# Optimization experiments

Hardware: AMD Instinct MI355X
Metric: run time of the kernel (lower is better)

## Reference

```python
import jax, jax.numpy as jnp
import numpy as np

EPS = 1e-6
B, T, J, D, H = 8, 512, 26, 256, 8
DH = D // H
HID = 4 * D


def logmap0(x):
    # x: [..., d+1] on hyperboloid (curvature -1). Tangent at origin -> [..., d]
    x0 = jnp.clip(x[..., :1], 1.0 + 1e-7, None)
    xs = x[..., 1:]
    n = jnp.maximum(jnp.linalg.norm(xs, axis=-1, keepdims=True), EPS)
    return jnp.arccosh(x0) * xs / n


def expmap0(v):
    # v: [..., d] tangent at origin -> [..., d+1] on hyperboloid
    n = jnp.maximum(jnp.linalg.norm(v, axis=-1, keepdims=True), EPS)
    return jnp.concatenate([jnp.cosh(n), jnp.sinh(n) * v / n], axis=-1)


def layernorm(v, g, b):
    m = jnp.mean(v, axis=-1, keepdims=True)
    var = jnp.var(v, axis=-1, keepdims=True)
    return (v - m) * jax.lax.rsqrt(var + 1e-5) * g + b


def lorentz_residual(x, z):
    # Lorentz centroid: normalize x+z so <m,m>_L = -1
    m = x + z
    mink = -m[..., :1] ** 2 + jnp.sum(m[..., 1:] ** 2, axis=-1, keepdims=True)
    return m / jnp.sqrt(jnp.clip(-mink, EPS, None))


def setup_inputs() -> dict:
    key = jax.random.key(0)
    ks = jax.random.split(key, 12)
    xs = jax.random.normal(ks[0], (B, T, J, D), jnp.float32) * 0.5
    x0 = jnp.sqrt(1.0 + jnp.sum(xs ** 2, axis=-1, keepdims=True))
    x = jnp.concatenate([x0, xs], axis=-1)  # valid points on H^d
    s = 1.0 / np.sqrt(D)
    inp = {
        "x": x,
        "g1": jnp.ones((D,), jnp.float32), "beta1": jnp.zeros((D,), jnp.float32),
        "Wq": jax.random.normal(ks[1], (D, D), jnp.float32) * s,
        "Wk": jax.random.normal(ks[2], (D, D), jnp.float32) * s,
        "Wv": jax.random.normal(ks[3], (D, D), jnp.float32) * s,
        "Wo": jax.random.normal(ks[4], (D, D), jnp.float32) * s,
        "bq": jnp.zeros((D,), jnp.float32), "bk": jnp.zeros((D,), jnp.float32),
        "bv": jnp.zeros((D,), jnp.float32), "bo": jnp.zeros((D,), jnp.float32),
        "g2": jnp.ones((D,), jnp.float32), "beta2": jnp.zeros((D,), jnp.float32),
        "W1": jax.random.normal(ks[5], (D, HID), jnp.float32) * s,
        "bf1": jnp.zeros((HID,), jnp.float32),
        "W2": jax.random.normal(ks[6], (HID, D), jnp.float32) * (1.0 / np.sqrt(HID)),
        "bf2": jnp.zeros((D,), jnp.float32),
    }
    return inp


def reference(x, g1, beta1, Wq, Wk, Wv, Wo, bq, bk, bv, bo, g2, beta2, W1, bf1, W2, bf2):
    # norm1: tangent-space LayerNorm
    u = layernorm(logmap0(x), g1, beta1)            # [B,T,J,D]
    xn = expmap0(u)
    # linear temporal attention (per joint, across T)
    t = logmap0(xn)
    q = (t @ Wq + bq).reshape(B, T, J, H, DH)
    k = (t @ Wk + bk).reshape(B, T, J, H, DH)
    v = (t @ Wv + bv).reshape(B, T, J, H, DH)
    pq = jax.nn.elu(q) + 1.0
    pk = jax.nn.elu(k) + 1.0
    kv = jnp.einsum('btjhk,btjhd->bjhkd', pk, v)    # O(T) global context
    ksum = jnp.sum(pk, axis=1)                      # [B,J,H,DH]
    num = jnp.einsum('btjhk,bjhkd->btjhd', pq, kv)
    den = jnp.einsum('btjhk,bjhk->btjh', pq, ksum)[..., None] + EPS
    o = (num / den).reshape(B, T, J, D) @ Wo + bo
    z = expmap0(o)
    # Lorentz (Minkowski) residual
    h = lorentz_residual(x, z)
    # norm2 + FFN in tangent space
    u2 = layernorm(logmap0(h), g2, beta2)
    f = jax.nn.gelu(u2 @ W1 + bf1) @ W2 + bf2
    return expmap0(f)
```

## Files before the change

kernel.cpp:

```cpp
#include <hip/hip_runtime.h>
#include <hip/hip_bf16.h>
#include <math.h>


#define EPSF 1e-6f
#define B_ 8
#define T_ 512
#define J_ 26
#define D_ 256
#define H_ 8
#define DH_ 32
#define HID_ 1024
#define NP1 257
#define R_ (B_*T_*J_)

typedef float  f32x4  __attribute__((ext_vector_type(4)));
typedef short  s16x8  __attribute__((ext_vector_type(8)));
typedef short  s16x4  __attribute__((ext_vector_type(4)));

__device__ __forceinline__ int rp_to_r(int rp) {
  int bj = rp >> 9, t = rp & 511;
  int b = bj / 26, j = bj - 26 * b;
  return (b * 512 + t) * 26 + j;
}

__device__ __forceinline__ void async16(const void* g, void* l) {
  __builtin_amdgcn_global_load_lds(
      (const __attribute__((address_space(1))) unsigned int*)g,
      (__attribute__((address_space(3))) unsigned int*)l, 16, 0, 0);
}

__device__ __forceinline__ float wave_sum(float v) {
#pragma unroll
  for (int m = 32; m; m >>= 1) v += __shfl_xor(v, m, 64);
  return v;
}

__global__ __launch_bounds__(256) void k_wconv(const float* __restrict__ W,
                                               __hip_bfloat16* __restrict__ Wt,
                                               int K, int N) {
  __shared__ float tile[32][33];
  int n0 = blockIdx.x * 32, k0 = blockIdx.y * 32;
  int tx = threadIdx.x, ty = threadIdx.y;
#pragma unroll
  for (int i = ty; i < 32; i += 8) tile[i][tx] = W[(size_t)(k0 + i) * N + n0 + tx];
  __syncthreads();
#pragma unroll
  for (int i = ty; i < 32; i += 8)
    Wt[(size_t)(n0 + i) * K + k0 + tx] = __float2bfloat16(tile[tx][i]);
}

__global__ __launch_bounds__(256) void k_t(const float* __restrict__ x,
                                           const float* __restrict__ g1,
                                           const float* __restrict__ beta1,
                                           __hip_bfloat16* __restrict__ t) {
  int rp = blockIdx.x * 4 + (threadIdx.x >> 6);
  int l = threadIdx.x & 63;
  int r = rp_to_r(rp);
  const float* xr = x + (size_t)r * NP1;
  float xs[4];
#pragma unroll
  for (int i = 0; i < 4; ++i) xs[i] = xr[1 + l + 64*i];
  float p1 = xs[0]+xs[1]+xs[2]+xs[3];
  float p2 = xs[0]*xs[0]+xs[1]*xs[1]+xs[2]*xs[2]+xs[3]*xs[3];
  float s1 = wave_sum(p1);
  float s2 = wave_sum(p2);
  float mean = s1 * (1.0f/256.0f);
  float var = s2 * (1.0f/256.0f) - mean*mean;
  float rstd = rsqrtf(var + 1e-5f);
#pragma unroll
  for (int i = 0; i < 4; ++i) {
    int c = l + 64*i;
    t[(size_t)rp * D_ + c] = __float2bfloat16((xs[i]-mean)*rstd*g1[c] + beta1[c]);
  }
}

#define PHASE(BUF, MH, NH, GIDX, DO_VM) {                                      \
    s16x8 af_[4][2]; s16x8 bf_[2][2];                                          \
    const char* ab_ = lds + ((BUF)*2+(MH))*16384;                              \
    const char* bb_ = lds + 65536 + ((BUF)*2+(NH))*16384;                      \
    _Pragma("unroll") for (int f_ = 0; f_ < 4; ++f_)                           \
      _Pragma("unroll") for (int ks_ = 0; ks_ < 2; ++ks_)                      \
        af_[f_][ks_] = *(const s16x8*)(ab_ + aoffs[f_][ks_]);                  \
    _Pragma("unroll") for (int ni_ = 0; ni_ < 2; ++ni_)                        \
      _Pragma("unroll") for (int ks_ = 0; ks_ < 2; ++ks_)                      \
        bf_[ni_][ks_] = *(const s16x8*)(bb_ + boffs[ni_][ks_]);                \
    STAGE_HALF((GIDX) + 6);                                                    \
    if (DO_VM) asm volatile("s_waitcnt vmcnt(4)" ::: "memory");                \
    asm volatile("s_barrier" ::: "memory");                                    \
    __builtin_amdgcn_sched_barrier(0);                                         \
    __builtin_amdgcn_s_setprio(1);                                             \
    _Pragma("unroll") for (int ks_ = 0; ks_ < 2; ++ks_)                        \
      _Pragma("unroll") for (int f_ = 0; f_ < 4; ++f_)                         \
        _Pragma("unroll") for (int ni_ = 0; ni_ < 2; ++ni_)                    \
          acc[(MH)*4+f_][(NH)*2+ni_] = __builtin_amdgcn_mfma_f32_16x16x32_bf16(\
              bf_[ni_][ks_], af_[f_][ks_], acc[(MH)*4+f_][(NH)*2+ni_], 0,0,0); \
    __builtin_amdgcn_s_setprio(0);                                             \
    asm volatile("s_barrier" ::: "memory");                                    \
  }

template<int ACT, int OUTF, int KDIM>
__global__ __launch_bounds__(512, 2) void k_gemm(const __hip_bfloat16* __restrict__ A,
                                                 const __hip_bfloat16* __restrict__ Bt,
                                                 const float* __restrict__ bias,
                                                 void* __restrict__ Cout,
                                                 int M, int N) {
  extern __shared__ char lds[];
  constexpr int NKT = KDIM / 64;
  int tid = threadIdx.x;
  int w = tid >> 6, l = tid & 63;
  int wr = w >> 2, wc = w & 3;
  int ml = l & 15, quad = l >> 4;
  int n0 = blockIdx.x * 256, m0 = blockIdx.y * 256;

  const short* Ag = (const short*)A + (size_t)m0 * KDIM;
  const short* Bg = (const short*)Bt + (size_t)n0 * KDIM;

  int srow = w*8 + (l >> 3);
  int scol = (((l & 7) ^ ((l >> 3) & 7)) * 8);

  auto STAGE_HALF = [&](int n) {
    if (n >= 4*NKT) return;
    int kt = n >> 2;
    int isB = n & 1, h = (n >> 1) & 1, buf = kt & 1;
    const short* src = isB ? Bg : Ag;
    const short* g0 = src + (size_t)(h*128 + srow) * KDIM + kt*64 + scol;
    char* dst = lds + isB*65536 + (buf*2 + h)*16384 + w*1024;
    async16(g0, dst);
    async16(g0 + (size_t)64 * KDIM, dst + 8192);
  };

  int aoffs[4][2], boffs[2][2];
#pragma unroll
  for (int f = 0; f < 4; ++f) {
    int r = wr*64 + f*16 + ml;
#pragma unroll
    for (int ks = 0; ks < 2; ++ks)
      aoffs[f][ks] = (r*128 + ks*64 + quad*16) ^ ((ml & 7) << 4);
  }
#pragma unroll
  for (int ni = 0; ni < 2; ++ni) {
    int rb = wc*32 + ni*16 + ml;
#pragma unroll
    for (int ks = 0; ks < 2; ++ks)
      boffs[ni][ks] = (rb*128 + ks*64 + quad*16) ^ ((ml & 7) << 4);
  }

  f32x4 acc[8][4];
#pragma unroll
  for (int i = 0; i < 8; ++i)
#pragma unroll
    for (int j = 0; j < 4; ++j) acc[i][j] = {0.f, 0.f, 0.f, 0.f};

#pragma unroll
  for (int n = 0; n < 6; ++n) STAGE_HALF(n);
  asm volatile("s_waitcnt vmcnt(4)" ::: "memory");
  asm volatile("s_barrier" ::: "memory");

  for (int cc = 0; cc < NKT/2; ++cc) {
    int g0 = cc * 8;
    PHASE(0, 0, 0, g0+0, 0)
    PHASE(0, 0, 1, g0+1, 0)
    PHASE(0, 1, 0, g0+2, 0)
    PHASE(0, 1, 1, g0+3, 1)
    PHASE(1, 0, 0, g0+4, 0)
    PHASE(1, 0, 1, g0+5, 0)
    PHASE(1, 1, 0, g0+6, 0)
    PHASE(1, 1, 1, g0+7, 1)
  }

#pragma unroll
  for (int mi = 0; mi < 8; ++mi) {
    size_t row = (size_t)(m0 + (mi>>2)*128 + wr*64 + (mi&3)*16 + ml);
#pragma unroll
    for (int nj = 0; nj < 4; ++nj) {
      int col = n0 + (nj>>1)*128 + wc*32 + (nj&1)*16 + quad*4;
      f32x4 bj = *(const f32x4*)&bias[col];
      f32x4 v = acc[mi][nj] + bj;
      if (ACT == 1) {
#pragma unroll
        for (int e = 0; e < 4; ++e) v[e] = (v[e] > 0.0f) ? v[e] + 1.0f : __expf(v[e]);
      } else if (ACT == 2) {
#pragma unroll
        for (int e = 0; e < 4; ++e) {
          float vv = v[e], v2 = vv * vv;
          float ex = __expf(vv * fmaf(v2, -0.0713548327f, -1.5957691216f));
          v[e] = vv * __builtin_amdgcn_rcpf(1.0f + ex);
        }
      }
      if (OUTF) {
        *(f32x4*)&((float*)Cout)[row * N + col] = v;
      } else {
        s16x4 sv;
#pragma unroll
        for (int e = 0; e < 4; ++e) {
          __hip_bfloat16 b = __float2bfloat16(v[e]);
          sv[e] = *(short*)&b;
        }
        *(s16x4*)&((__hip_bfloat16*)Cout)[row * N + col] = sv;
      }
    }
  }
}

__global__ __launch_bounds__(256) void k_kv(const __hip_bfloat16* __restrict__ pk,
                                            const __hip_bfloat16* __restrict__ v,
                                            float* __restrict__ kv,
                                            float* __restrict__ ksum) {
  __shared__ float spk[2][64*36];
  __shared__ float sv [2][64*33];
  __shared__ float sks[8][32];
  int blk = blockIdx.x;
  int h = blk & 7, bj = blk >> 3;
  int tid = threadIdx.x;
  int tq = tid >> 2;
  int qc = tid & 3;
  int kgrp = tid >> 5;
  int dd = tid & 31;

  const short* pkg = (const short*)pk + (size_t)bj * 512 * 256 + h*32 + qc*8;
  const short* vg  = (const short*)v  + (size_t)bj * 512 * 256 + h*32 + qc*8;

  float acc[4] = {0.f, 0.f, 0.f, 0.f};
  float ks = 0.f;
  s16x8 rp_, rv_;

  auto GLOAD = [&](int c) {
    size_t off = (size_t)(c*64 + tq) * 256;
    rp_ = *(const s16x8*)(pkg + off);
    rv_ = *(const s16x8*)(vg + off);
  };
  auto DSWRITE = [&](int c) {
    int bsel = c & 1;
    float* prow = &spk[bsel][tq*36];
    float* vrow = &sv[bsel][tq*33];
#pragma unroll
    for (int e = 0; e < 8; ++e) {
      unsigned up = ((unsigned)(unsigned short)rp_[e]) << 16;
      unsigned uv = ((unsigned)(unsigned short)rv_[e]) << 16;
      prow[e*4 + qc]  = __uint_as_float(up);
      vrow[qc*8 + e]  = __uint_as_float(uv);
    }
  };
  auto COMPUTE = [&](int c) {
    int bsel = c & 1;
    const float* pb = &spk[bsel][kgrp*4];
    const float* vb = &sv[bsel][dd];
#pragma unroll
    for (int t = 0; t < 64; ++t) {
      f32x4 pf = *(const f32x4*)(pb + t*36);
      float vv = vb[t*33];
#pragma unroll
      for (int m = 0; m < 4; ++m) acc[m] = fmaf(pf[m], vv, acc[m]);
    }
    const float* kb = &spk[bsel][kgrp*8*36 + ((dd&7)<<2) + (dd>>3)];
#pragma unroll
    for (int i = 0; i < 8; ++i) ks += kb[i*36];
  };

  GLOAD(0);
#pragma unroll 2
  for (int c = 0; c < 8; ++c) {
    DSWRITE(c);
    if (c < 7) GLOAD(c + 1);
    __syncthreads();
    COMPUTE(c);
  }

  float* kvp = kv + (size_t)blk * 1024;
#pragma unroll
  for (int m = 0; m < 4; ++m) kvp[(kgrp + 8*m)*32 + dd] = acc[m];

  sks[kgrp][dd] = ks;
  __syncthreads();
  if (tid < 32) {
    float s = 0.f;
#pragma unroll
    for (int g = 0; g < 8; ++g) s += sks[g][tid];
    ksum[(size_t)blk * 32 + tid] = s;
  }
}

__global__ __launch_bounds__(256) void k_attn(const __hip_bfloat16* __restrict__ pq,
                                              const float* __restrict__ kv,
                                              const float* __restrict__ ksum,
                                              __hip_bfloat16* __restrict__ attn) {
  __shared__ float psf[32][264];
  __shared__ float dens[32][8];
  int bj = blockIdx.y;
  int t0 = blockIdx.x * 32;
  int g0 = bj * 512 + t0;
  int tid = threadIdx.x, w = tid >> 6, l = tid & 63;
  int h = w*2 + (l >> 5), dd = l & 31;

  const float* kvp = kv + ((size_t)bj * 8 + h) * (DH_*DH_);
  float kvreg[32];
#pragma unroll
  for (int k = 0; k < 32; ++k) kvreg[k] = kvp[k*32 + dd];

  for (int tr = 0; tr < 32; ++tr)
    psf[tr][tid] = __bfloat162float(pq[(size_t)(g0 + tr) * D_ + tid]);
  __syncthreads();

  {
    int tr = tid & 31, hh = tid >> 5;
    const float* ksp = ksum + ((size_t)bj * 8 + hh) * DH_;
    float dsum = 0.f;
#pragma unroll
    for (int k = 0; k < 32; ++k) dsum = fmaf(psf[tr][hh*32 + k], ksp[k], dsum);
    dens[tr][hh] = dsum;
  }
  __syncthreads();

  for (int tr = 0; tr < 32; ++tr) {
    const float* pr = &psf[tr][h*32];
    float num = 0.f;
#pragma unroll
    for (int k = 0; k < 32; ++k) num = fmaf(pr[k], kvreg[k], num);
    float rden = __builtin_amdgcn_rcpf(dens[tr][h] + EPSF);
    attn[(size_t)(g0 + tr) * D_ + tid] = __float2bfloat16(num * rden);
  }
}

__global__ __launch_bounds__(256) void k_u2(const __hip_bfloat16* __restrict__ o,
                                            const float* __restrict__ x,
                                            const float* __restrict__ g2,
                                            const float* __restrict__ beta2,
                                            __hip_bfloat16* __restrict__ u2) {
  int rp = blockIdx.x * 4 + (threadIdx.x >> 6);
  int l = threadIdx.x & 63;
  int r = rp_to_r(rp);
  const float* xr = x + (size_t)r * NP1;
  float ov[4], xs[4];
#pragma unroll
  for (int i = 0; i < 4; ++i) {
    ov[i] = __bfloat162float(o[(size_t)rp * D_ + l + 64*i]);
    xs[i] = xr[1 + l + 64*i];
  }
  float p2 = ov[0]*ov[0]+ov[1]*ov[1]+ov[2]*ov[2]+ov[3]*ov[3];
  float s2o = wave_sum(p2);
  float no = fmaxf(sqrtf(s2o), EPSF);
  float e = __expf(no);
  float c = (e - 1.0f/e) * 0.5f / no;
  float mi[4];
#pragma unroll
  for (int i = 0; i < 4; ++i) mi[i] = xs[i] + c * ov[i];
  float q1 = mi[0]+mi[1]+mi[2]+mi[3];
  float q2 = mi[0]*mi[0]+mi[1]*mi[1]+mi[2]*mi[2]+mi[3]*mi[3];
  float s1 = wave_sum(q1);
  float s2 = wave_sum(q2);
  float mean = s1 * (1.0f/256.0f);
  float var = s2 * (1.0f/256.0f) - mean*mean;
  float rstd = rsqrtf(var + 1e-5f);
#pragma unroll
  for (int i = 0; i < 4; ++i) {
    int cc = l + 64*i;
    u2[(size_t)rp * D_ + cc] = __float2bfloat16((mi[i]-mean)*rstd*g2[cc] + beta2[cc]);
  }
}

__global__ __launch_bounds__(256) void k_out(const float* __restrict__ f,
                                             float* __restrict__ out) {
  int rp = blockIdx.x * 4 + (threadIdx.x >> 6);
  int l = threadIdx.x & 63;
  int r = rp_to_r(rp);
  const float* fr = f + (size_t)rp * D_;
  float fv[4];
#pragma unroll
  for (int i = 0; i < 4; ++i) fv[i] = fr[l + 64*i];
  float p2 = fv[0]*fv[0]+fv[1]*fv[1]+fv[2]*fv[2]+fv[3]*fv[3];
  float s2 = wave_sum(p2);
  float n = fmaxf(sqrtf(s2), EPSF);
  float e = __expf(n);
  float ie = 1.0f / e;
  float sh = (e - ie) * 0.5f;
  float ch = (e + ie) * 0.5f;
  float s = sh / n;
  float* orow = out + (size_t)r * NP1;
  if (l == 0) orow[0] = ch;
#pragma unroll
  for (int i = 0; i < 4; ++i) orow[1 + l + 64*i] = s * fv[i];
}

extern "C" void kernel_launch(void* const* d_in, const int* in_sizes, int n_in,
                              void* d_out, int out_size, void* d_ws, size_t ws_size,
                              hipStream_t stream) {
  const float* x     = (const float*)d_in[0];
  const float* g1    = (const float*)d_in[1];
  const float* beta1 = (const float*)d_in[2];
  const float* Wq    = (const float*)d_in[3];
  const float* Wk    = (const float*)d_in[4];
  const float* Wv    = (const float*)d_in[5];
  const float* Wo    = (const float*)d_in[6];
  const float* bq    = (const float*)d_in[7];
  const float* bk    = (const float*)d_in[8];
  const float* bv    = (const float*)d_in[9];
  const float* bo    = (const float*)d_in[10];
  const float* g2    = (const float*)d_in[11];
  const float* beta2 = (const float*)d_in[12];
  const float* W1    = (const float*)d_in[13];
  const float* bf1   = (const float*)d_in[14];
  const float* W2    = (const float*)d_in[15];
  const float* bf2   = (const float*)d_in[16];
  float* out = (float*)d_out;
  char* ws = (char*)d_ws;

  size_t off = 0;
  __hip_bfloat16* wqT = (__hip_bfloat16*)(ws + off); off += (size_t)D_*D_*2;
  __hip_bfloat16* wkT = (__hip_bfloat16*)(ws + off); off += (size_t)D_*D_*2;
  __hip_bfloat16* wvT = (__hip_bfloat16*)(ws + off); off += (size_t)D_*D_*2;
  __hip_bfloat16* woT = (__hip_bfloat16*)(ws + off); off += (size_t)D_*D_*2;
  __hip_bfloat16* w1T = (__hip_bfloat16*)(ws + off); off += (size_t)HID_*D_*2;
  __hip_bfloat16* w2T = (__hip_bfloat16*)(ws + off); off += (size_t)D_*HID_*2;
  float* kvb = (float*)(ws + off); off += (size_t)(B_*J_*H_)*(DH_*DH_)*4;
  float* ksb = (float*)(ws + off); off += (size_t)(B_*J_*H_)*DH_*4;
  off = (off + 255) & ~(size_t)255;
  __hip_bfloat16* tb = (__hip_bfloat16*)(ws + off); off += (size_t)R_*D_*2;
  __hip_bfloat16* qb = (__hip_bfloat16*)(ws + off); off += (size_t)R_*D_*2;
  __hip_bfloat16* kb = (__hip_bfloat16*)(ws + off); off += (size_t)R_*D_*2;
  __hip_bfloat16* vb = (__hip_bfloat16*)(ws + off); off += (size_t)R_*D_*2;
  __hip_bfloat16* hid = (__hip_bfloat16*)(ws + off); off += (size_t)(R_/2)*HID_*2;
  float* fbuf = (float*)qb;

  static bool attr_done = false;
  if (!attr_done) {
    hipFuncSetAttribute((const void*)k_gemm<1,0,256>,  hipFuncAttributeMaxDynamicSharedMemorySize, 131072);
    hipFuncSetAttribute((const void*)k_gemm<0,0,256>,  hipFuncAttributeMaxDynamicSharedMemorySize, 131072);
    hipFuncSetAttribute((const void*)k_gemm<2,0,256>,  hipFuncAttributeMaxDynamicSharedMemorySize, 131072);
    hipFuncSetAttribute((const void*)k_gemm<0,1,1024>, hipFuncAttributeMaxDynamicSharedMemorySize, 131072);
    attr_done = true;
  }

  dim3 tconv(32, 8);
  k_wconv<<<dim3(D_/32,  D_/32),  tconv, 0, stream>>>(Wq, wqT, D_,  D_);
  k_wconv<<<dim3(D_/32,  D_/32),  tconv, 0, stream>>>(Wk, wkT, D_,  D_);
  k_wconv<<<dim3(D_/32,  D_/32),  tconv, 0, stream>>>(Wv, wvT, D_,  D_);
  k_wconv<<<dim3(D_/32,  D_/32),  tconv, 0, stream>>>(Wo, woT, D_,  D_);
  k_wconv<<<dim3(HID_/32, D_/32), tconv, 0, stream>>>(W1, w1T, D_,  HID_);
  k_wconv<<<dim3(D_/32, HID_/32), tconv, 0, stream>>>(W2, w2T, HID_, D_);

  k_t<<<R_/4, 256, 0, stream>>>(x, g1, beta1, tb);

  dim3 gqkv(D_/256, R_/256);
  k_gemm<1,0,256><<<gqkv, 512, 131072, stream>>>(tb, wqT, bq, qb, R_, D_);
  k_gemm<1,0,256><<<gqkv, 512, 131072, stream>>>(tb, wkT, bk, kb, R_, D_);
  k_gemm<0,0,256><<<gqkv, 512, 131072, stream>>>(tb, wvT, bv, vb, R_, D_);

  k_kv<<<B_*J_*H_, 256, 0, stream>>>(kb, vb, kvb, ksb);
  k_attn<<<dim3(T_/32, B_*J_), 256, 0, stream>>>(qb, kvb, ksb, kb);

  k_gemm<0,0,256><<<gqkv, 512, 131072, stream>>>(kb, woT, bo, vb, R_, D_);
  k_u2<<<R_/4, 256, 0, stream>>>(vb, x, g2, beta2, tb);

  const int Rc = R_ / 2;
  for (int c = 0; c < 2; ++c) {
    k_gemm<2,0,256><<<dim3(HID_/256, Rc/256), 512, 131072, stream>>>(
        tb + (size_t)c * Rc * D_, w1T, bf1, hid, Rc, HID_);
    k_gemm<0,1,1024><<<dim3(D_/256, Rc/256), 512, 131072, stream>>>(
        hid, w2T, bf2, fbuf + (size_t)c * Rc * D_, Rc, D_);
  }

  k_out<<<R_/4, 256, 0, stream>>>(fbuf, out);
}
```

Before: 802.7 us.

## Fuse final expmap0 into FFN2 GEMM epilogue and simplify k_kv tiling

The final expmap0 (row norm, cosh/sinh scaling, scatter into the 257-wide output) moves into the W2 GEMM epilogue, using a cross-wave LDS reduction of row norms. This removes the fp32 intermediate buffer round trip and the separate k_out launch. The k_kv kernel is also rewritten to use 32-row chunks with a simpler LDS layout and a direct ksum computation. The fused epilogue writes strided, unvectorized scalar stores to the output, and the k_kv rewrite adds more barriers per iteration.

Result: faster. 782.2 us (-2.6%).

```diff
diff --git a/kernel.cpp b/kernel.cpp
--- a/kernel.cpp
+++ b/kernel.cpp
@@ -13,6 +13,8 @@
 #define HID_ 1024
 #define NP1 257
 #define R_ (B_*T_*J_)
+#define NBJ (B_*J_)
+#define NBH (NBJ*H_)
 
 typedef float  f32x4  __attribute__((ext_vector_type(4)));
 typedef short  s16x8  __attribute__((ext_vector_type(8)));
@@ -99,12 +101,12 @@
     asm volatile("s_barrier" ::: "memory");                                    \
   }
 
-template<int ACT, int OUTF, int KDIM>
+template<int ACT, int EPI, int KDIM>
 __global__ __launch_bounds__(512, 2) void k_gemm(const __hip_bfloat16* __restrict__ A,
                                                  const __hip_bfloat16* __restrict__ Bt,
                                                  const float* __restrict__ bias,
                                                  void* __restrict__ Cout,
-                                                 int M, int N) {
+                                                 int M, int N, int mOff) {
   extern __shared__ char lds[];
   constexpr int NKT = KDIM / 64;
   int tid = threadIdx.x;
@@ -169,28 +171,26 @@
     PHASE(1, 1, 1, g0+7, 1)
   }
 
-#pragma unroll
-  for (int mi = 0; mi < 8; ++mi) {
-    size_t row = (size_t)(m0 + (mi>>2)*128 + wr*64 + (mi&3)*16 + ml);
-#pragma unroll
-    for (int nj = 0; nj < 4; ++nj) {
-      int col = n0 + (nj>>1)*128 + wc*32 + (nj&1)*16 + quad*4;
-      f32x4 bj = *(const f32x4*)&bias[col];
-      f32x4 v = acc[mi][nj] + bj;
-      if (ACT == 1) {
-#pragma unroll
-        for (int e = 0; e < 4; ++e) v[e] = (v[e] > 0.0f) ? v[e] + 1.0f : __expf(v[e]);
-      } else if (ACT == 2) {
-#pragma unroll
-        for (int e = 0; e < 4; ++e) {
-          float vv = v[e], v2 = vv * vv;
-          float ex = __expf(vv * fmaf(v2, -0.0713548327f, -1.5957691216f));
-          v[e] = vv * __builtin_amdgcn_rcpf(1.0f + ex);
+  if (EPI == 0) {
+#pragma unroll
+    for (int mi = 0; mi < 8; ++mi) {
+      size_t row = (size_t)(m0 + (mi>>2)*128 + wr*64 + (mi&3)*16 + ml);
+#pragma unroll
+      for (int nj = 0; nj < 4; ++nj) {
+        int col = n0 + (nj>>1)*128 + wc*32 + (nj&1)*16 + quad*4;
+        f32x4 bj = *(const f32x4*)&bias[col];
+        f32x4 v = acc[mi][nj] + bj;
+        if (ACT == 1) {
+#pragma unroll
+          for (int e = 0; e < 4; ++e) v[e] = (v[e] > 0.0f) ? v[e] + 1.0f : __expf(v[e]);
+        } else if (ACT == 2) {
+#pragma unroll
+          for (int e = 0; e < 4; ++e) {
+            float vv = v[e], v2 = vv * vv;
+            float ex = __expf(vv * fmaf(v2, -0.0713548327f, -1.5957691216f));
+            v[e] = vv * __builtin_amdgcn_rcpf(1.0f + ex);
+          }
         }
-      }
-      if (OUTF) {
-        *(f32x4*)&((float*)Cout)[row * N + col] = v;
-      } else {
         s16x4 sv;
 #pragma unroll
         for (int e = 0; e < 4; ++e) {
@@ -200,6 +200,61 @@
         *(s16x4*)&((__hip_bfloat16*)Cout)[row * N + col] = sv;
       }
     }
+  } else {
+    float* out = (float*)Cout;
+    float* red = (float*)lds;
+    f32x4 bj4[4];
+#pragma unroll
+    for (int nj = 0; nj < 4; ++nj)
+      bj4[nj] = *(const f32x4*)&bias[(nj>>1)*128 + wc*32 + (nj&1)*16 + quad*4];
+    float n2[8];
+#pragma unroll
+    for (int mi = 0; mi < 8; ++mi) {
+      float p = 0.f;
+#pragma unroll
+      for (int nj = 0; nj < 4; ++nj)
+#pragma unroll
+        for (int e = 0; e < 4; ++e) {
+          float f = acc[mi][nj][e] + bj4[nj][e];
+          p = fmaf(f, f, p);
+        }
+      p += __shfl_xor(p, 16, 64);
+      p += __shfl_xor(p, 32, 64);
+      n2[mi] = p;
+    }
+    __syncthreads();
+    if (quad == 0) {
+#pragma unroll
+      for (int mi = 0; mi < 8; ++mi)
+        red[((wr*4 + wc)*8 + mi)*16 + ml] = n2[mi];
+    }
+    __syncthreads();
+#pragma unroll
+    for (int mi = 0; mi < 8; ++mi) {
+      float s = 0.f;
+#pragma unroll
+      for (int w2 = 0; w2 < 4; ++w2)
+        s += red[((wr*4 + w2)*8 + mi)*16 + ml];
+      n2[mi] = s;
+    }
+#pragma unroll
+    for (int mi = 0; mi < 8; ++mi) {
+      int rowp = m0 + (mi>>2)*128 + wr*64 + (mi&3)*16 + ml;
+      int r = rp_to_r(mOff + rowp);
+      float* orow = out + (size_t)r * NP1;
+      float n = fmaxf(sqrtf(n2[mi]), EPSF);
+      float e = __expf(n);
+      float ie = 1.0f / e;
+      float sc = (e - ie) * 0.5f / n;
+      if (wc == 0 && quad == 0) orow[0] = (e + ie) * 0.5f;
+#pragma unroll
+      for (int nj = 0; nj < 4; ++nj) {
+        int col = (nj>>1)*128 + wc*32 + (nj&1)*16 + quad*4;
+#pragma unroll
+        for (int e2 = 0; e2 < 4; ++e2)
+          orow[1 + col + e2] = sc * (acc[mi][nj][e2] + bj4[nj][e2]);
+      }
+    }
   }
 }
 
@@ -207,78 +262,56 @@
                                             const __hip_bfloat16* __restrict__ v,
                                             float* __restrict__ kv,
                                             float* __restrict__ ksum) {
-  __shared__ float spk[2][64*36];
-  __shared__ float sv [2][64*33];
-  __shared__ float sks[8][32];
+  __shared__ float spk[32][32];
+  __shared__ float sv [32][32];
   int blk = blockIdx.x;
   int h = blk & 7, bj = blk >> 3;
   int tid = threadIdx.x;
-  int tq = tid >> 2;
-  int qc = tid & 3;
-  int kgrp = tid >> 5;
-  int dd = tid & 31;
-
-  const short* pkg = (const short*)pk + (size_t)bj * 512 * 256 + h*32 + qc*8;
-  const short* vg  = (const short*)v  + (size_t)bj * 512 * 256 + h*32 + qc*8;
+  int row = tid >> 3, cg = tid & 7;
+  int k0 = tid >> 5, dd = tid & 31;
+
+  const short* pkg = (const short*)pk + (size_t)bj*512*256 + h*32 + cg*4;
+  const short* vg  = (const short*)v  + (size_t)bj*512*256 + h*32 + cg*4;
+
+  s16x4 rp_, rv_;
+  auto GLOAD = [&](int c) {
+    size_t off = (size_t)(c*32 + row) * 256;
+    rp_ = *(const s16x4*)(pkg + off);
+    rv_ = *(const s16x4*)(vg + off);
+  };
 
   float acc[4] = {0.f, 0.f, 0.f, 0.f};
   float ks = 0.f;
-  s16x8 rp_, rv_;
-
-  auto GLOAD = [&](int c) {
-    size_t off = (size_t)(c*64 + tq) * 256;
-    rp_ = *(const s16x8*)(pkg + off);
-    rv_ = *(const s16x8*)(vg + off);
-  };
-  auto DSWRITE = [&](int c) {
-    int bsel = c & 1;
-    float* prow = &spk[bsel][tq*36];
-    float* vrow = &sv[bsel][tq*33];
-#pragma unroll
-    for (int e = 0; e < 8; ++e) {
-      unsigned up = ((unsigned)(unsigned short)rp_[e]) << 16;
-      unsigned uv = ((unsigned)(unsigned short)rv_[e]) << 16;
-      prow[e*4 + qc]  = __uint_as_float(up);
-      vrow[qc*8 + e]  = __uint_as_float(uv);
-    }
-  };
-  auto COMPUTE = [&](int c) {
-    int bsel = c & 1;
-    const float* pb = &spk[bsel][kgrp*4];
-    const float* vb = &sv[bsel][dd];
-#pragma unroll
-    for (int t = 0; t < 64; ++t) {
-      f32x4 pf = *(const f32x4*)(pb + t*36);
-      float vv = vb[t*33];
-#pragma unroll
-      for (int m = 0; m < 4; ++m) acc[m] = fmaf(pf[m], vv, acc[m]);
-    }
-    const float* kb = &spk[bsel][kgrp*8*36 + ((dd&7)<<2) + (dd>>3)];
-#pragma unroll
-    for (int i = 0; i < 8; ++i) ks += kb[i*36];
-  };
 
   GLOAD(0);
-#pragma unroll 2
-  for (int c = 0; c < 8; ++c) {
-    DSWRITE(c);
-    if (c < 7) GLOAD(c + 1);
+  for (int c = 0; c < 16; ++c) {
+    f32x4 pf, vf;
+#pragma unroll
+    for (int e = 0; e < 4; ++e) {
+      pf[e] = __uint_as_float(((unsigned)(unsigned short)rp_[e]) << 16);
+      vf[e] = __uint_as_float(((unsigned)(unsigned short)rv_[e]) << 16);
+    }
+    *(f32x4*)&spk[row][cg*4] = pf;
+    *(f32x4*)&sv [row][cg*4] = vf;
     __syncthreads();
-    COMPUTE(c);
+    if (c < 15) GLOAD(c + 1);
+#pragma unroll
+    for (int q = 0; q < 32; ++q) {
+      float vv = sv[q][dd];
+#pragma unroll
+      for (int m = 0; m < 4; ++m) acc[m] = fmaf(spk[q][k0 + 8*m], vv, acc[m]);
+    }
+    if (tid < 32) {
+#pragma unroll
+      for (int q = 0; q < 32; ++q) ks += spk[q][tid];
+    }
+    __syncthreads();
   }
 
   float* kvp = kv + (size_t)blk * 1024;
 #pragma unroll
-  for (int m = 0; m < 4; ++m) kvp[(kgrp + 8*m)*32 + dd] = acc[m];
-
-  sks[kgrp][dd] = ks;
-  __syncthreads();
-  if (tid < 32) {
-    float s = 0.f;
-#pragma unroll
-    for (int g = 0; g < 8; ++g) s += sks[g][tid];
-    ksum[(size_t)blk * 32 + tid] = s;
-  }
+  for (int m = 0; m < 4; ++m) kvp[(k0 + 8*m)*32 + dd] = acc[m];
+  if (tid < 32) ksum[(size_t)blk * 32 + tid] = ks;
 }
 
 __global__ __launch_bounds__(256) void k_attn(const __hip_bfloat16* __restrict__ pq,
@@ -357,29 +390,6 @@
     int cc = l + 64*i;
     u2[(size_t)rp * D_ + cc] = __float2bfloat16((mi[i]-mean)*rstd*g2[cc] + beta2[cc]);
   }
-}
-
-__global__ __launch_bounds__(256) void k_out(const float* __restrict__ f,
-                                             float* __restrict__ out) {
-  int rp = blockIdx.x * 4 + (threadIdx.x >> 6);
-  int l = threadIdx.x & 63;
-  int r = rp_to_r(rp);
-  const float* fr = f + (size_t)rp * D_;
-  float fv[4];
-#pragma unroll
-  for (int i = 0; i < 4; ++i) fv[i] = fr[l + 64*i];
-  float p2 = fv[0]*fv[0]+fv[1]*fv[1]+fv[2]*fv[2]+fv[3]*fv[3];
-  float s2 = wave_sum(p2);
-  float n = fmaxf(sqrtf(s2), EPSF);
-  float e = __expf(n);
-  float ie = 1.0f / e;
-  float sh = (e - ie) * 0.5f;
-  float ch = (e + ie) * 0.5f;
-  float s = sh / n;
-  float* orow = out + (size_t)r * NP1;
-  if (l == 0) orow[0] = ch;
-#pragma unroll
-  for (int i = 0; i < 4; ++i) orow[1 + l + 64*i] = s * fv[i];
 }
 
 extern "C" void kernel_launch(void* const* d_in, const int* in_sizes, int n_in,
@@ -412,22 +422,21 @@
   __hip_bfloat16* woT = (__hip_bfloat16*)(ws + off); off += (size_t)D_*D_*2;
   __hip_bfloat16* w1T = (__hip_bfloat16*)(ws + off); off += (size_t)HID_*D_*2;
   __hip_bfloat16* w2T = (__hip_bfloat16*)(ws + off); off += (size_t)D_*HID_*2;
-  float* kvb = (float*)(ws + off); off += (size_t)(B_*J_*H_)*(DH_*DH_)*4;
-  float* ksb = (float*)(ws + off); off += (size_t)(B_*J_*H_)*DH_*4;
+  float* kvb = (float*)(ws + off); off += (size_t)NBH*(DH_*DH_)*4;
+  float* ksb = (float*)(ws + off); off += (size_t)NBH*DH_*4;
   off = (off + 255) & ~(size_t)255;
   __hip_bfloat16* tb = (__hip_bfloat16*)(ws + off); off += (size_t)R_*D_*2;
   __hip_bfloat16* qb = (__hip_bfloat16*)(ws + off); off += (size_t)R_*D_*2;
   __hip_bfloat16* kb = (__hip_bfloat16*)(ws + off); off += (size_t)R_*D_*2;
   __hip_bfloat16* vb = (__hip_bfloat16*)(ws + off); off += (size_t)R_*D_*2;
   __hip_bfloat16* hid = (__hip_bfloat16*)(ws + off); off += (size_t)(R_/2)*HID_*2;
-  float* fbuf = (float*)qb;
 
   static bool attr_done = false;
   if (!attr_done) {
     hipFuncSetAttribute((const void*)k_gemm<1,0,256>,  hipFuncAttributeMaxDynamicSharedMemorySize, 131072);
     hipFuncSetAttribute((const void*)k_gemm<0,0,256>,  hipFuncAttributeMaxDynamicSharedMemorySize, 131072);
     hipFuncSetAttribute((const void*)k_gemm<2,0,256>,  hipFuncAttributeMaxDynamicSharedMemorySize, 131072);
-    hipFuncSetAttribute((const void*)k_gemm<0,1,1024>, hipFuncAttributeMaxDynamicSharedMemorySize, 131072);
+    hipFuncSetAttribute((const void*)k_gemm<0,2,1024>, hipFuncAttributeMaxDynamicSharedMemorySize, 131072);
     attr_done = true;
   }
 
@@ -442,23 +451,21 @@
   k_t<<<R_/4, 256, 0, stream>>>(x, g1, beta1, tb);
 
   dim3 gqkv(D_/256, R_/256);
-  k_gemm<1,0,256><<<gqkv, 512, 131072, stream>>>(tb, wqT, bq, qb, R_, D_);
-  k_gemm<1,0,256><<<gqkv, 512, 131072, stream>>>(tb, wkT, bk, kb, R_, D_);
-  k_gemm<0,0,256><<<gqkv, 512, 131072, stream>>>(tb, wvT, bv, vb, R_, D_);
-
-  k_kv<<<B_*J_*H_, 256, 0, stream>>>(kb, vb, kvb, ksb);
-  k_attn<<<dim3(T_/32, B_*J_), 256, 0, stream>>>(qb, kvb, ksb, kb);
-
-  k_gemm<0,0,256><<<gqkv, 512, 131072, stream>>>(kb, woT, bo, vb, R_, D_);
+  k_gemm<1,0,256><<<gqkv, 512, 131072, stream>>>(tb, wqT, bq, qb, R_, D_, 0);
+  k_gemm<1,0,256><<<gqkv, 512, 131072, stream>>>(tb, wkT, bk, kb, R_, D_, 0);
+  k_gemm<0,0,256><<<gqkv, 512, 131072, stream>>>(tb, wvT, bv, vb, R_, D_, 0);
+
+  k_kv<<<NBH, 256, 0, stream>>>(kb, vb, kvb, ksb);
+  k_attn<<<dim3(T_/32, NBJ), 256, 0, stream>>>(qb, kvb, ksb, kb);
+
+  k_gemm<0,0,256><<<gqkv, 512, 131072, stream>>>(kb, woT, bo, vb, R_, D_, 0);
   k_u2<<<R_/4, 256, 0, stream>>>(vb, x, g2, beta2, tb);
 
   const int Rc = R_ / 2;
   for (int c = 0; c < 2; ++c) {
     k_gemm<2,0,256><<<dim3(HID_/256, Rc/256), 512, 131072, stream>>>(
-        tb + (size_t)c * Rc * D_, w1T, bf1, hid, Rc, HID_);
-    k_gemm<0,1,1024><<<dim3(D_/256, Rc/256), 512, 131072, stream>>>(
-        hid, w2T, bf2, fbuf + (size_t)c * Rc * D_, Rc, D_);
-  }
-
-  k_out<<<R_/4, 256, 0, stream>>>(fbuf, out);
-}
+        tb + (size_t)c * Rc * D_, w1T, bf1, hid, Rc, HID_, 0);
+    k_gemm<0,2,1024><<<dim3(1, Rc/256), 512, 131072, stream>>>(
+        hid, w2T, bf2, out, Rc, D_, c * Rc);
+  }
+}
```
